# Performance work log

Measured on AMD Instinct MI355X. Metric: run time of the kernel, lower is better.

Reference implementation:

```python
import jax, jax.numpy as jnp
import numpy as np
from functools import partial

EPS = 1e-5
GROUPS = 32
RK4_STEPS = 8


def group_norm(x, g, b):
    B, C, H, W = x.shape
    xr = x.reshape(B, GROUPS, C // GROUPS, H, W)
    m = xr.mean(axis=(2, 3, 4), keepdims=True)
    v = xr.var(axis=(2, 3, 4), keepdims=True)
    xn = ((xr - m) * jax.lax.rsqrt(v + EPS)).reshape(B, C, H, W)
    return xn * g[None, :, None, None] + b[None, :, None, None]


def conv3x3(x, w, b):
    y = jax.lax.conv_general_dilated(x, w, (1, 1), ((1, 1), (1, 1)),
                                     dimension_numbers=('NCHW', 'OIHW', 'NCHW'))
    return y + b[None, :, None, None]


def concat_conv3x3(t, x, w, b):
    # ConcatConv2d: append a constant time channel, then 3x3 conv
    B, _, H, W = x.shape
    tt = jnp.full((B, 1, H, W), t, dtype=x.dtype)
    return conv3x3(jnp.concatenate([tt, x], axis=1), w, b)


def atten_init_fwd(x, p):
    out = jax.nn.relu(group_norm(x, p['ai_g1'], p['ai_b1']))
    out = conv3x3(out, p['ai_w'], p['ai_cb'])
    out = jax.nn.relu(group_norm(out, p['ai_g2'], p['ai_b2']))
    return group_norm(out, p['ai_g3'], p['ai_b3'])


def odefunc(t, x, p):
    out = jax.nn.relu(group_norm(x, p['of_g1'], p['of_b1']))
    out = concat_conv3x3(t, out, p['of_w1'], p['of_cb1'])
    out = jax.nn.relu(group_norm(out, p['of_g2'], p['of_b2']))
    out = concat_conv3x3(t, out, p['of_w2'], p['of_cb2'])
    return group_norm(out, p['of_g3'], p['of_b3'])


def rk4(f, y0, t0, t1, n):
    h = jnp.asarray((t1 - t0) / n, dtype=y0.dtype)
    def step(carry, _):
        y, t = carry
        k1 = f(t, y)
        k2 = f(t + 0.5 * h, y + 0.5 * h * k1)
        k3 = f(t + 0.5 * h, y + 0.5 * h * k2)
        k4 = f(t + h, y + h * k3)
        y = y + (h / 6.0) * (k1 + 2.0 * k2 + 2.0 * k3 + k4)
        return (y, t + h), None
    (y, _), _ = jax.lax.scan(step, (y0, jnp.asarray(t0, y0.dtype)), None, length=n)
    return y


def setup_inputs() -> dict:
    key = jax.random.key(0)
    dim = 32
    B, H, W = 128, 64, 64
    ks = jax.random.split(key, 8)
    d = {
        'x': jax.random.normal(ks[0], (B, dim, H, W), dtype=jnp.float32),
        # atten_init params
        'ai_g1': jnp.ones((dim,), jnp.float32), 'ai_b1': jnp.zeros((dim,), jnp.float32),
        'ai_w': jax.random.normal(ks[1], (dim, dim, 3, 3), jnp.float32) * 0.05,
        'ai_cb': jnp.zeros((dim,), jnp.float32),
        'ai_g2': jnp.ones((dim,), jnp.float32), 'ai_b2': jnp.zeros((dim,), jnp.float32),
        'ai_g3': jnp.ones((dim,), jnp.float32), 'ai_b3': jnp.zeros((dim,), jnp.float32),
        # odefunc params (ConcatConv2d: in_channels = dim + 1 time channel)
        'of_g1': jnp.ones((dim,), jnp.float32), 'of_b1': jnp.zeros((dim,), jnp.float32),
        'of_w1': jax.random.normal(ks[2], (dim, dim + 1, 3, 3), jnp.float32) * 0.05,
        'of_cb1': jnp.zeros((dim,), jnp.float32),
        'of_g2': jnp.ones((dim,), jnp.float32), 'of_b2': jnp.zeros((dim,), jnp.float32),
        'of_w2': jax.random.normal(ks[3], (dim, dim + 1, 3, 3), jnp.float32) * 0.05,
        'of_cb2': jnp.zeros((dim,), jnp.float32),
        'of_g3': jnp.ones((dim,), jnp.float32), 'of_b3': jnp.zeros((dim,), jnp.float32),
    }
    return d


def reference(x, ai_g1, ai_b1, ai_w, ai_cb, ai_g2, ai_b2, ai_g3, ai_b3,
              of_g1, of_b1, of_w1, of_cb1, of_g2, of_b2, of_w2, of_cb2,
              of_g3, of_b3):
    p = dict(ai_g1=ai_g1, ai_b1=ai_b1, ai_w=ai_w, ai_cb=ai_cb, ai_g2=ai_g2,
             ai_b2=ai_b2, ai_g3=ai_g3, ai_b3=ai_b3, of_g1=of_g1, of_b1=of_b1,
             of_w1=of_w1, of_cb1=of_cb1, of_g2=of_g2, of_b2=of_b2, of_w2=of_w2,
             of_cb2=of_cb2, of_g3=of_g3, of_b3=of_b3)
    a0 = atten_init_fwd(x, p)
    x0 = jnp.concatenate([x, a0], axis=0)  # torch.cat default dim=0
    f = lambda t, y: odefunc(t, y, p)
    out1 = rk4(f, x0, 0.0, 1.0, RK4_STEPS)  # odeint(...)[1]
    return out1
```

## Files before the change

kernel.cpp:

```cpp
#include <hip/hip_runtime.h>

#define HW 4096
#define CIN 32

typedef __bf16 bf16x8 __attribute__((ext_vector_type(8)));
typedef float  f32x4  __attribute__((ext_vector_type(4)));
typedef unsigned short ushort8_v __attribute__((ext_vector_type(8)));

__device__ __forceinline__ unsigned short f2b(float f) {
    __bf16 b = (__bf16)f;
    return __builtin_bit_cast(unsigned short, b);
}
__device__ __forceinline__ float b2f(unsigned short s) {
    unsigned int u = ((unsigned int)s) << 16;
    return __builtin_bit_cast(float, u);
}
__device__ __forceinline__ bf16x8 ld_frag(const unsigned short* p) {
    ushort8_v u = *(const ushort8_v*)p;
    return __builtin_bit_cast(bf16x8, u);
}

__global__ __launch_bounds__(256)
void prep_kernel(const float* __restrict__ ai_w,
                 const float* __restrict__ of_w1,
                 const float* __restrict__ of_w2,
                 unsigned short* __restrict__ wp_ai,
                 unsigned short* __restrict__ wp1,
                 unsigned short* __restrict__ wp2,
                 float* __restrict__ tc1, float* __restrict__ tc2)
{
    const int t = threadIdx.x;
    for (int i = t; i < 9 * 32 * 40; i += 256) {
        const int s = i / 1280;
        const int rem = i - s * 1280;
        const int oc = rem / 40;
        const int ci = rem - oc * 40;
        unsigned short va = 0, v1 = 0, v2 = 0;
        if (ci < 32) {
            va = f2b(ai_w[(oc * 32 + ci) * 9 + s]);
            v1 = f2b(of_w1[(oc * 33 + ci + 1) * 9 + s]);
            v2 = f2b(of_w2[(oc * 33 + ci + 1) * 9 + s]);
        }
        wp_ai[i] = va; wp1[i] = v1; wp2[i] = v2;
    }
    for (int i = t; i < 32 * 9; i += 256) {
        const int oc = i / 9;
        const int cls = i - oc * 9;
        const int rc = cls / 3, cc = cls - rc * 3;
        float s1 = 0.f, s2 = 0.f;
        for (int ky = 0; ky < 3; ++ky) {
            if ((rc == 0 && ky == 0) || (rc == 2 && ky == 2)) continue;
            for (int kx = 0; kx < 3; ++kx) {
                if ((cc == 0 && kx == 0) || (cc == 2 && kx == 2)) continue;
                s1 += of_w1[(oc * 33) * 9 + ky * 3 + kx];
                s2 += of_w2[(oc * 33) * 9 + ky * 3 + kx];
            }
        }
        tc1[i] = s1; tc2[i] = s2;
    }
}

__global__ __launch_bounds__(256)
void xstat_kernel(const float* __restrict__ x, float* __restrict__ y,
                  unsigned short* __restrict__ xb,
                  const float* __restrict__ g_ai, const float* __restrict__ b_ai,
                  const float* __restrict__ g_of, const float* __restrict__ b_of,
                  float* __restrict__ st_ai, float* __restrict__ st_of)
{
    const int p = blockIdx.x;
    const int c = p & 31;
    const int t = threadIdx.x;
    const float4* ip = (const float4*)(x + (size_t)p * HW);
    float4* yp = (float4*)(y + (size_t)p * HW);
    ushort4* xp = (ushort4*)(xb + (size_t)p * HW);
    float s = 0.f, ss = 0.f;
#pragma unroll
    for (int i = 0; i < 4; ++i) {
        const float4 q = ip[t + i * 256];
        yp[t + i * 256] = q;
        ushort4 u; u.x = f2b(q.x); u.y = f2b(q.y); u.z = f2b(q.z); u.w = f2b(q.w);
        xp[t + i * 256] = u;
        s += q.x + q.y + q.z + q.w;
        ss += q.x * q.x + q.y * q.y + q.z * q.z + q.w * q.w;
    }
#pragma unroll
    for (int off = 32; off > 0; off >>= 1) {
        s  += __shfl_xor(s, off);
        ss += __shfl_xor(ss, off);
    }
    __shared__ float red[8];
    const int wid = t >> 6;
    if ((t & 63) == 0) { red[wid] = s; red[4 + wid] = ss; }
    __syncthreads();
    if (t == 0) {
        s  = red[0] + red[1] + red[2] + red[3];
        ss = red[4] + red[5] + red[6] + red[7];
        const float mean = s * (1.f / HW);
        const float var  = ss * (1.f / HW) - mean * mean;
        const float rstd = rsqrtf(var + 1e-5f);
        const float sa = g_ai[c] * rstd;
        st_ai[p * 2]     = sa;
        st_ai[p * 2 + 1] = b_ai[c] - mean * sa;
        const float so = g_of[c] * rstd;
        st_of[p * 2]     = so;
        st_of[p * 2 + 1] = b_of[c] - mean * so;
    }
}

template<int HAS_TIME, int STATS, int OUT_BF16, int FIN>
__global__ __launch_bounds__(512)
void conv_kernel(const unsigned short* __restrict__ in, void* __restrict__ outv,
                 const float* __restrict__ st,
                 const float* __restrict__ fg, const float* __restrict__ fb,
                 const unsigned short* __restrict__ wp,
                 const float* __restrict__ cb, const float* __restrict__ tcls,
                 float tval, float* __restrict__ straw)
{
    const int blk = blockIdx.x;
    const int b  = blk >> 3;
    const int hb = blk & 7;
    const int h0 = hb * 8;
    const int t  = threadIdx.x;
    const int l  = t & 63;
    const int wid = t >> 6;
    const int lm = l & 15;
    const int lg = l >> 4;

    __shared__ unsigned short tile[10 * 66 * 40];
    __shared__ float sst[64];

    if (FIN) {
        float s = 0.f, ss = 0.f;
        if (t < 256) {
            const float2 pr = ((const float2*)st)[(size_t)(b * 32 + (t >> 3)) * 8 + (t & 7)];
            s = pr.x; ss = pr.y;
        }
        s += __shfl_xor(s, 1); ss += __shfl_xor(ss, 1);
        s += __shfl_xor(s, 2); ss += __shfl_xor(ss, 2);
        s += __shfl_xor(s, 4); ss += __shfl_xor(ss, 4);
        if (t < 256 && (t & 7) == 0) {
            const int ci = t >> 3;
            const float mean = s * (1.f / HW);
            const float var  = ss * (1.f / HW) - mean * mean;
            const float rstd = rsqrtf(var + 1e-5f);
            const float sc = fg[ci] * rstd;
            sst[ci * 2]     = sc;
            sst[ci * 2 + 1] = fb[ci] - mean * sc;
        }
    } else {
        if (t < 64) sst[t] = st[b * 64 + t];
    }

    bf16x8 wreg[2][9];
    {
        const unsigned short* wb = wp + (size_t)(lm * 40 + 8 * lg);
#pragma unroll
        for (int nt = 0; nt < 2; ++nt)
#pragma unroll
            for (int s = 0; s < 9; ++s)
                wreg[nt][s] = ld_frag(wb + s * 1280 + nt * 640);
    }
    __syncthreads();

    const unsigned short* inb = in + (size_t)b * (CIN * HW);
#pragma unroll
    for (int tau = t; tau < 640; tau += 512) {
        const int g = tau / 160;
        const int rem = tau - g * 160;
        const int r = rem >> 4;
        const int wq = rem & 15;
        const int hh = h0 - 1 + r;
        unsigned short* dst = &tile[(r * 66 + wq * 4 + 1) * 40 + 8 * g];
        if (hh >= 0 && hh < 64) {
            const unsigned short* src = inb + (size_t)(8 * g) * HW + hh * 64 + wq * 4;
            ushort4 U[8];
#pragma unroll
            for (int j = 0; j < 8; ++j) U[j] = *(const ushort4*)(src + (size_t)j * HW);
            float scv[8], shv[8];
#pragma unroll
            for (int j = 0; j < 8; ++j) {
                const float2 s2 = *(const float2*)(&sst[(8 * g + j) * 2]);
                scv[j] = s2.x; shv[j] = s2.y;
            }
#pragma unroll
            for (int k = 0; k < 4; ++k) {
                ushort8_v F;
#pragma unroll
                for (int j = 0; j < 8; ++j) {
                    const unsigned short e = ((const unsigned short*)&U[j])[k];
                    F[j] = f2b(fmaxf(b2f(e) * scv[j] + shv[j], 0.f));
                }
                *(ushort8_v*)(dst + k * 40) = F;
            }
        } else {
            const ushort8_v z = {0, 0, 0, 0, 0, 0, 0, 0};
#pragma unroll
            for (int k = 0; k < 4; ++k) *(ushort8_v*)(dst + k * 40) = z;
        }
    }
    if (t < 80) {
        const int g = t & 3;
        const int rr = t >> 2;
        const int r = rr >> 1;
        const int col = (rr & 1) ? 65 : 0;
        const ushort8_v z = {0, 0, 0, 0, 0, 0, 0, 0};
        *(ushort8_v*)&tile[(r * 66 + col) * 40 + 8 * g] = z;
    }
    __syncthreads();

    f32x4 acc[4][2];
#pragma unroll
    for (int mt = 0; mt < 4; ++mt)
#pragma unroll
        for (int nt = 0; nt < 2; ++nt) acc[mt][nt] = (f32x4){0.f, 0.f, 0.f, 0.f};

#pragma unroll
    for (int ky = 0; ky < 3; ++ky)
#pragma unroll
        for (int kx = 0; kx < 3; ++kx) {
            const int s = ky * 3 + kx;
            const int base = ((wid + ky) * 66 + kx + lm) * 40 + 8 * lg;
#pragma unroll
            for (int mt = 0; mt < 4; ++mt) {
                const bf16x8 a = ld_frag(&tile[base + mt * 640]);
                acc[mt][0] = __builtin_amdgcn_mfma_f32_16x16x32_bf16(a, wreg[0][s], acc[mt][0], 0, 0, 0);
                acc[mt][1] = __builtin_amdgcn_mfma_f32_16x16x32_bf16(a, wreg[1][s], acc[mt][1], 0, 0, 0);
            }
        }

    const int h = h0 + wid;
    const int rc = (h == 0) ? 0 : ((h == 63) ? 2 : 1);
    float bias_[2], tcn[2], tc0[2], tc2[2];
#pragma unroll
    for (int nt = 0; nt < 2; ++nt) {
        const int oc = nt * 16 + lm;
        bias_[nt] = cb[oc];
        if (HAS_TIME) {
            tcn[nt] = tcls[oc * 9 + rc * 3 + 1];
            tc0[nt] = tcls[oc * 9 + rc * 3 + 0];
            tc2[nt] = tcls[oc * 9 + rc * 3 + 2];
        }
    }
    float sl[2] = {0.f, 0.f}, ssl[2] = {0.f, 0.f};
    float* outf = (float*)outv;
    unsigned short* outb = (unsigned short*)outv;
#pragma unroll
    for (int mt = 0; mt < 4; ++mt) {
#pragma unroll
        for (int nt = 0; nt < 2; ++nt) {
            const int oc = nt * 16 + lm;
            float v[4];
#pragma unroll
            for (int r = 0; r < 4; ++r) {
                v[r] = acc[mt][nt][r] + bias_[nt];
                if (HAS_TIME) v[r] += tval * tcn[nt];
            }
            if (HAS_TIME && mt == 0 && lg == 0) v[0] += tval * (tc0[nt] - tcn[nt]);
            if (HAS_TIME && mt == 3 && lg == 3) v[3] += tval * (tc2[nt] - tcn[nt]);
            const int w0 = mt * 16 + lg * 4;
            const size_t o = ((size_t)(b * 32 + oc)) * HW + (size_t)h * 64 + w0;
            if (OUT_BF16) {
                ushort4 u;
                u.x = f2b(v[0]); u.y = f2b(v[1]); u.z = f2b(v[2]); u.w = f2b(v[3]);
                *(ushort4*)&outb[o] = u;
                if (STATS) {
#pragma unroll
                    for (int r = 0; r < 4; ++r) {
                        const float vr = b2f(f2b(v[r]));
                        sl[nt] += vr; ssl[nt] += vr * vr;
                    }
                }
            } else {
                float4 q; q.x = v[0]; q.y = v[1]; q.z = v[2]; q.w = v[3];
                *(float4*)&outf[o] = q;
                if (STATS) {
#pragma unroll
                    for (int r = 0; r < 4; ++r) { sl[nt] += v[r]; ssl[nt] += v[r] * v[r]; }
                }
            }
        }
    }
    if (STATS) {
        float s0 = sl[0], q0 = ssl[0], s1 = sl[1], q1 = ssl[1];
        s0 += __shfl_xor(s0, 16); s0 += __shfl_xor(s0, 32);
        q0 += __shfl_xor(q0, 16); q0 += __shfl_xor(q0, 32);
        s1 += __shfl_xor(s1, 16); s1 += __shfl_xor(s1, 32);
        q1 += __shfl_xor(q1, 16); q1 += __shfl_xor(q1, 32);
        __syncthreads();
        float* red = (float*)tile;
        if (lg == 0) {
            red[wid * 32 + lm]       = s0;  red[256 + wid * 32 + lm]       = q0;
            red[wid * 32 + 16 + lm]  = s1;  red[256 + wid * 32 + 16 + lm]  = q1;
        }
        __syncthreads();
        if (t < 32) {
            float S = 0.f, Q = 0.f;
#pragma unroll
            for (int w = 0; w < 8; ++w) { S += red[w * 32 + t]; Q += red[256 + w * 32 + t]; }
            float* dst = straw + ((size_t)(b * 32 + t) * 8 + hb) * 2;
            dst[0] = S; dst[1] = Q;
        }
    }
}

__global__ __launch_bounds__(256)
void dgn_kernel(const float* __restrict__ in, float* __restrict__ out,
                unsigned short* __restrict__ xbout,
                const float* __restrict__ g2, const float* __restrict__ b2,
                const float* __restrict__ g3, const float* __restrict__ b3,
                const float* __restrict__ g1n, const float* __restrict__ b1n,
                float* __restrict__ stout)
{
    const int p = blockIdx.x;
    const int c = p & 31;
    const int t = threadIdx.x;
    const float4* ip = (const float4*)(in + (size_t)p * HW);
    float4* op = (float4*)(out + (size_t)p * HW);
    ushort4* xp = (ushort4*)(xbout + (size_t)p * HW);
    __shared__ float red[8];
    const int wid = t >> 6;

    float4 v[4];
    float s = 0.f, ss = 0.f;
#pragma unroll
    for (int i = 0; i < 4; ++i) {
        float4 q = ip[t + i * 256];
        v[i] = q;
        s += q.x + q.y + q.z + q.w;
        ss += q.x * q.x + q.y * q.y + q.z * q.z + q.w * q.w;
    }
#pragma unroll
    for (int off = 32; off > 0; off >>= 1) {
        s  += __shfl_xor(s, off);
        ss += __shfl_xor(ss, off);
    }
    if ((t & 63) == 0) { red[wid] = s; red[4 + wid] = ss; }
    __syncthreads();
    s  = red[0] + red[1] + red[2] + red[3];
    ss = red[4] + red[5] + red[6] + red[7];
    float mean = s * (1.f / HW);
    float var  = ss * (1.f / HW) - mean * mean;
    float rstd = rsqrtf(var + 1e-5f);
    float sc = g2[c] * rstd;
    float sh = b2[c] - mean * sc;

    s = 0.f; ss = 0.f;
#pragma unroll
    for (int i = 0; i < 4; ++i) {
        float4 q = v[i];
        q.x = fmaxf(q.x * sc + sh, 0.f); q.y = fmaxf(q.y * sc + sh, 0.f);
        q.z = fmaxf(q.z * sc + sh, 0.f); q.w = fmaxf(q.w * sc + sh, 0.f);
        v[i] = q;
        s += q.x + q.y + q.z + q.w;
        ss += q.x * q.x + q.y * q.y + q.z * q.z + q.w * q.w;
    }
#pragma unroll
    for (int off = 32; off > 0; off >>= 1) {
        s  += __shfl_xor(s, off);
        ss += __shfl_xor(ss, off);
    }
    __syncthreads();
    if ((t & 63) == 0) { red[wid] = s; red[4 + wid] = ss; }
    __syncthreads();
    s  = red[0] + red[1] + red[2] + red[3];
    ss = red[4] + red[5] + red[6] + red[7];
    mean = s * (1.f / HW);
    var  = ss * (1.f / HW) - mean * mean;
    rstd = rsqrtf(var + 1e-5f);
    sc = g3[c] * rstd;
    sh = b3[c] - mean * sc;

    float s3 = 0.f, ss3 = 0.f;
#pragma unroll
    for (int i = 0; i < 4; ++i) {
        float4 q = v[i];
        q.x = q.x * sc + sh; q.y = q.y * sc + sh;
        q.z = q.z * sc + sh; q.w = q.w * sc + sh;
        op[t + i * 256] = q;
        ushort4 u; u.x = f2b(q.x); u.y = f2b(q.y); u.z = f2b(q.z); u.w = f2b(q.w);
        xp[t + i * 256] = u;
        s3 += q.x + q.y + q.z + q.w;
        ss3 += q.x * q.x + q.y * q.y + q.z * q.z + q.w * q.w;
    }
#pragma unroll
    for (int off = 32; off > 0; off >>= 1) {
        s3  += __shfl_xor(s3, off);
        ss3 += __shfl_xor(ss3, off);
    }
    __syncthreads();
    if ((t & 63) == 0) { red[wid] = s3; red[4 + wid] = ss3; }
    __syncthreads();
    if (t == 0) {
        s3  = red[0] + red[1] + red[2] + red[3];
        ss3 = red[4] + red[5] + red[6] + red[7];
        const float m3 = s3 * (1.f / HW);
        const float v3 = ss3 * (1.f / HW) - m3 * m3;
        const float r3 = rsqrtf(v3 + 1e-5f);
        const float sc1 = g1n[c] * r3;
        stout[p * 2]     = sc1;
        stout[p * 2 + 1] = b1n[c] - m3 * sc1;
    }
}

template<int MODE>
__global__ __launch_bounds__(256)
void gnrk_kernel(const unsigned short* __restrict__ kin,
                 const float* __restrict__ straw,
                 const float* __restrict__ g, const float* __restrict__ bt,
                 float* __restrict__ y, float* __restrict__ acc,
                 float ca, float cy,
                 const float* __restrict__ g1n, const float* __restrict__ b1n,
                 float* __restrict__ stout, unsigned short* __restrict__ xb,
                 unsigned short* __restrict__ yb)
{
    const int p = blockIdx.x;
    const int c = p & 31;
    const int t = threadIdx.x;

    const float2 pr = ((const float2*)straw)[(size_t)p * 8 + (t & 7)];
    float s = pr.x, ss = pr.y;
    s += __shfl_xor(s, 1); ss += __shfl_xor(ss, 1);
    s += __shfl_xor(s, 2); ss += __shfl_xor(ss, 2);
    s += __shfl_xor(s, 4); ss += __shfl_xor(ss, 4);
    const float mean = s * (1.f / HW);
    const float var  = ss * (1.f / HW) - mean * mean;
    const float rstd = rsqrtf(var + 1e-5f);
    const float sc = g[c] * rstd;
    const float sh = bt[c] - mean * sc;

    const ushort4* kp = (const ushort4*)(kin + (size_t)p * HW);
    const f32x4* ypl = (const f32x4*)(y + (size_t)p * HW);
    f32x4* yps = (f32x4*)(y + (size_t)p * HW);
    f32x4* ap  = (f32x4*)(acc + (size_t)p * HW);
    ushort4* xp = (ushort4*)(xb + (size_t)p * HW);
    ushort4* ybp = (ushort4*)(yb + (size_t)p * HW);
    __shared__ float red[8];
    const int wid = t >> 6;

    ushort4 ku[4];
#pragma unroll
    for (int i = 0; i < 4; ++i) ku[i] = kp[t + i * 256];
    f32x4 yv[4];
    if (MODE == 0) {
#pragma unroll
        for (int i = 0; i < 4; ++i)
            yv[i] = __builtin_nontemporal_load(ypl + t + i * 256);
    }
    ushort4 ybv[4];
    if (MODE == 1) {
#pragma unroll
        for (int i = 0; i < 4; ++i) ybv[i] = ybp[t + i * 256];
    }
    f32x4 av[4];
    if (MODE != 0) {
#pragma unroll
        for (int i = 0; i < 4; ++i) av[i] = ap[t + i * 256];
    }

    float s2 = 0.f, ss2 = 0.f;
#pragma unroll
    for (int i = 0; i < 4; ++i) {
        const int idx = t + i * 256;
        f32x4 kq;
        kq[0] = b2f(ku[i].x) * sc + sh; kq[1] = b2f(ku[i].y) * sc + sh;
        kq[2] = b2f(ku[i].z) * sc + sh; kq[3] = b2f(ku[i].w) * sc + sh;
        ushort4 u;
        if (MODE == 0) {
            f32x4 a, w;
#pragma unroll
            for (int j = 0; j < 4; ++j) {
                a[j] = yv[i][j] + ca * kq[j];
                w[j] = yv[i][j] + cy * kq[j];
            }
            ap[idx] = a;
            u.x = f2b(w[0]); u.y = f2b(w[1]); u.z = f2b(w[2]); u.w = f2b(w[3]);
            xp[idx] = u;
            ushort4 yu;
            yu.x = f2b(yv[i][0]); yu.y = f2b(yv[i][1]);
            yu.z = f2b(yv[i][2]); yu.w = f2b(yv[i][3]);
            ybp[idx] = yu;
        } else if (MODE == 1) {
            f32x4 a, w;
            a[0] = av[i][0] + ca * kq[0]; a[1] = av[i][1] + ca * kq[1];
            a[2] = av[i][2] + ca * kq[2]; a[3] = av[i][3] + ca * kq[3];
            w[0] = b2f(ybv[i].x) + cy * kq[0]; w[1] = b2f(ybv[i].y) + cy * kq[1];
            w[2] = b2f(ybv[i].z) + cy * kq[2]; w[3] = b2f(ybv[i].w) + cy * kq[3];
            ap[idx] = a;
            u.x = f2b(w[0]); u.y = f2b(w[1]); u.z = f2b(w[2]); u.w = f2b(w[3]);
            xp[idx] = u;
        } else {
            f32x4 w;
            w[0] = av[i][0] + ca * kq[0]; w[1] = av[i][1] + ca * kq[1];
            w[2] = av[i][2] + ca * kq[2]; w[3] = av[i][3] + ca * kq[3];
            __builtin_nontemporal_store(w, yps + idx);
            u.x = f2b(w[0]); u.y = f2b(w[1]); u.z = f2b(w[2]); u.w = f2b(w[3]);
            xp[idx] = u;
        }
        const float r0 = b2f(u.x), r1 = b2f(u.y), r2 = b2f(u.z), r3 = b2f(u.w);
        s2  += r0 + r1 + r2 + r3;
        ss2 += r0 * r0 + r1 * r1 + r2 * r2 + r3 * r3;
    }
#pragma unroll
    for (int off = 32; off > 0; off >>= 1) {
        s2  += __shfl_xor(s2, off);
        ss2 += __shfl_xor(ss2, off);
    }
    if ((t & 63) == 0) { red[wid] = s2; red[4 + wid] = ss2; }
    __syncthreads();
    if (t == 0) {
        s2  = red[0] + red[1] + red[2] + red[3];
        ss2 = red[4] + red[5] + red[6] + red[7];
        const float m2 = s2 * (1.f / HW);
        const float v2 = ss2 * (1.f / HW) - m2 * m2;
        const float r2 = rsqrtf(v2 + 1e-5f);
        const float sc1 = g1n[c] * r2;
        stout[p * 2]     = sc1;
        stout[p * 2 + 1] = b1n[c] - m2 * sc1;
    }
}

extern "C" void kernel_launch(void* const* d_in, const int* in_sizes, int n_in,
                              void* d_out, int out_size, void* d_ws, size_t ws_size,
                              hipStream_t stream) {
    (void)in_sizes; (void)n_in; (void)out_size; (void)ws_size;
    const float* x      = (const float*)d_in[0];
    const float* ai_g1  = (const float*)d_in[1];
    const float* ai_b1  = (const float*)d_in[2];
    const float* ai_w   = (const float*)d_in[3];
    const float* ai_cb  = (const float*)d_in[4];
    const float* ai_g2  = (const float*)d_in[5];
    const float* ai_b2  = (const float*)d_in[6];
    const float* ai_g3  = (const float*)d_in[7];
    const float* ai_b3  = (const float*)d_in[8];
    const float* of_g1  = (const float*)d_in[9];
    const float* of_b1  = (const float*)d_in[10];
    const float* of_w1  = (const float*)d_in[11];
    const float* of_cb1 = (const float*)d_in[12];
    const float* of_g2  = (const float*)d_in[13];
    const float* of_b2  = (const float*)d_in[14];
    const float* of_w2  = (const float*)d_in[15];
    const float* of_cb2 = (const float*)d_in[16];
    const float* of_g3  = (const float*)d_in[17];
    const float* of_b3  = (const float*)d_in[18];

    float* y = (float*)d_out;
    const size_t N  = (size_t)256 * 32 * 64 * 64;
    const size_t NH = N / 2;
    float* ws = (float*)d_ws;
    float* ACC = ws;
    float* YTf = ws;
    unsigned short* Abf = (unsigned short*)(ws + N);
    unsigned short* XB  = (unsigned short*)(ws + N + N / 2);
    unsigned short* YTB = (unsigned short*)(ws + 2 * N);
    unsigned short* YB  = (unsigned short*)(ws + 2 * N + N / 2);
    float* tail  = ws + 3 * N;
    float* ST1    = tail;               tail += 16384;
    float* ST_AI  = tail;               tail += 8192;
    float* STRAW1 = tail;               tail += 131072;
    float* STRAW2 = tail;               tail += 131072;
    unsigned short* WPai = (unsigned short*)tail;  tail += 5760;
    unsigned short* WP1  = (unsigned short*)tail;  tail += 5760;
    unsigned short* WP2  = (unsigned short*)tail;  tail += 5760;
    float* TC1  = tail;                 tail += 288;
    float* TC2  = tail;                 tail += 288;

    const float h = 0.125f;

    prep_kernel<<<1, 256, 0, stream>>>(ai_w, of_w1, of_w2, WPai, WP1, WP2, TC1, TC2);

    xstat_kernel<<<4096, 256, 0, stream>>>(x, y, XB, ai_g1, ai_b1, of_g1, of_b1,
                                           ST_AI, ST1);
    conv_kernel<0, 0, 0, 0><<<1024, 512, 0, stream>>>(XB, YTf, ST_AI, nullptr, nullptr,
                                                      WPai, ai_cb, nullptr, 0.f, nullptr);
    dgn_kernel<<<4096, 256, 0, stream>>>(YTf, y + NH, XB + NH, ai_g2, ai_b2,
                                         ai_g3, ai_b3, of_g1, of_b1, ST1 + 8192);

    auto eval = [&](float tv, float ca, float cy, int mode) {
        conv_kernel<1, 1, 1, 0><<<2048, 512, 0, stream>>>(XB, Abf, ST1, nullptr, nullptr,
                                                          WP1, of_cb1, TC1, tv, STRAW1);
        conv_kernel<1, 1, 1, 1><<<2048, 512, 0, stream>>>(Abf, YTB, STRAW1, of_g2, of_b2,
                                                          WP2, of_cb2, TC2, tv, STRAW2);
        if (mode == 0)
            gnrk_kernel<0><<<8192, 256, 0, stream>>>(YTB, STRAW2, of_g3, of_b3, y, ACC,
                                                     ca, cy, of_g1, of_b1, ST1, XB, YB);
        else if (mode == 1)
            gnrk_kernel<1><<<8192, 256, 0, stream>>>(YTB, STRAW2, of_g3, of_b3, y, ACC,
                                                     ca, cy, of_g1, of_b1, ST1, XB, YB);
        else
            gnrk_kernel<2><<<8192, 256, 0, stream>>>(YTB, STRAW2, of_g3, of_b3, y, ACC,
                                                     ca, cy, of_g1, of_b1, ST1, XB, YB);
    };

    for (int s = 0; s < 8; ++s) {
        const float t0 = h * (float)s;
        eval(t0,            h / 6.f, 0.5f * h, 0);
        eval(t0 + 0.5f * h, h / 3.f, 0.5f * h, 1);
        eval(t0 + 0.5f * h, h / 3.f, h,        1);
        eval(t0 + h,        h / 6.f, 0.f,      2);
    }
}
```

Measured before the change: 5.493 ms.

## Store RK4 increment accumulator in bf16 and keep y bf16 copy from prior step

The RK4 accumulator moves from an fp32 buffer holding y+sum to a bf16 buffer holding only the weighted sum of k terms, with y added back in fp32 at the final stage. The bf16 copy of y is now produced by the previous final stage (and by the init kernels) instead of in mode 0. Mode 0 no longer reads the fp32 y, so only mode 2 touches fp32 y, which cuts global memory traffic in the bandwidth-bound elementwise kernels and shrinks the workspace. In exchange, increments are rounded to bf16 in the accumulator, which risks accuracy.

```diff
diff --git a/kernel.cpp b/kernel.cpp
--- a/kernel.cpp
+++ b/kernel.cpp
@@ -62,7 +62,7 @@
 
 __global__ __launch_bounds__(256)
 void xstat_kernel(const float* __restrict__ x, float* __restrict__ y,
-                  unsigned short* __restrict__ xb,
+                  unsigned short* __restrict__ xb, unsigned short* __restrict__ yb,
                   const float* __restrict__ g_ai, const float* __restrict__ b_ai,
                   const float* __restrict__ g_of, const float* __restrict__ b_of,
                   float* __restrict__ st_ai, float* __restrict__ st_of)
@@ -73,6 +73,7 @@
     const float4* ip = (const float4*)(x + (size_t)p * HW);
     float4* yp = (float4*)(y + (size_t)p * HW);
     ushort4* xp = (ushort4*)(xb + (size_t)p * HW);
+    ushort4* ybp = (ushort4*)(yb + (size_t)p * HW);
     float s = 0.f, ss = 0.f;
 #pragma unroll
     for (int i = 0; i < 4; ++i) {
@@ -80,6 +81,7 @@
         yp[t + i * 256] = q;
         ushort4 u; u.x = f2b(q.x); u.y = f2b(q.y); u.z = f2b(q.z); u.w = f2b(q.w);
         xp[t + i * 256] = u;
+        ybp[t + i * 256] = u;
         s += q.x + q.y + q.z + q.w;
         ss += q.x * q.x + q.y * q.y + q.z * q.z + q.w * q.w;
     }
@@ -305,7 +307,7 @@
 
 __global__ __launch_bounds__(256)
 void dgn_kernel(const float* __restrict__ in, float* __restrict__ out,
-                unsigned short* __restrict__ xbout,
+                unsigned short* __restrict__ xbout, unsigned short* __restrict__ ybout,
                 const float* __restrict__ g2, const float* __restrict__ b2,
                 const float* __restrict__ g3, const float* __restrict__ b3,
                 const float* __restrict__ g1n, const float* __restrict__ b1n,
@@ -317,6 +319,7 @@
     const float4* ip = (const float4*)(in + (size_t)p * HW);
     float4* op = (float4*)(out + (size_t)p * HW);
     ushort4* xp = (ushort4*)(xbout + (size_t)p * HW);
+    ushort4* ybp = (ushort4*)(ybout + (size_t)p * HW);
     __shared__ float red[8];
     const int wid = t >> 6;
 
@@ -379,6 +382,7 @@
         op[t + i * 256] = q;
         ushort4 u; u.x = f2b(q.x); u.y = f2b(q.y); u.z = f2b(q.z); u.w = f2b(q.w);
         xp[t + i * 256] = u;
+        ybp[t + i * 256] = u;
         s3 += q.x + q.y + q.z + q.w;
         ss3 += q.x * q.x + q.y * q.y + q.z * q.z + q.w * q.w;
     }
@@ -407,7 +411,7 @@
 void gnrk_kernel(const unsigned short* __restrict__ kin,
                  const float* __restrict__ straw,
                  const float* __restrict__ g, const float* __restrict__ bt,
-                 float* __restrict__ y, float* __restrict__ acc,
+                 float* __restrict__ y, unsigned short* __restrict__ db,
                  float ca, float cy,
                  const float* __restrict__ g1n, const float* __restrict__ b1n,
                  float* __restrict__ stout, unsigned short* __restrict__ xb,
@@ -431,8 +435,8 @@
     const ushort4* kp = (const ushort4*)(kin + (size_t)p * HW);
     const f32x4* ypl = (const f32x4*)(y + (size_t)p * HW);
     f32x4* yps = (f32x4*)(y + (size_t)p * HW);
-    f32x4* ap  = (f32x4*)(acc + (size_t)p * HW);
-    ushort4* xp = (ushort4*)(xb + (size_t)p * HW);
+    ushort4* dp  = (ushort4*)(db + (size_t)p * HW);
+    ushort4* xp  = (ushort4*)(xb + (size_t)p * HW);
     ushort4* ybp = (ushort4*)(yb + (size_t)p * HW);
     __shared__ float red[8];
     const int wid = t >> 6;
@@ -440,21 +444,21 @@
     ushort4 ku[4];
 #pragma unroll
     for (int i = 0; i < 4; ++i) ku[i] = kp[t + i * 256];
+    ushort4 ybv[4];
+    if (MODE != 2) {
+#pragma unroll
+        for (int i = 0; i < 4; ++i) ybv[i] = ybp[t + i * 256];
+    }
+    ushort4 dv[4];
+    if (MODE != 0) {
+#pragma unroll
+        for (int i = 0; i < 4; ++i) dv[i] = dp[t + i * 256];
+    }
     f32x4 yv[4];
-    if (MODE == 0) {
+    if (MODE == 2) {
 #pragma unroll
         for (int i = 0; i < 4; ++i)
             yv[i] = __builtin_nontemporal_load(ypl + t + i * 256);
-    }
-    ushort4 ybv[4];
-    if (MODE == 1) {
-#pragma unroll
-        for (int i = 0; i < 4; ++i) ybv[i] = ybp[t + i * 256];
-    }
-    f32x4 av[4];
-    if (MODE != 0) {
-#pragma unroll
-        for (int i = 0; i < 4; ++i) av[i] = ap[t + i * 256];
     }
 
     float s2 = 0.f, ss2 = 0.f;
@@ -465,36 +469,32 @@
         kq[0] = b2f(ku[i].x) * sc + sh; kq[1] = b2f(ku[i].y) * sc + sh;
         kq[2] = b2f(ku[i].z) * sc + sh; kq[3] = b2f(ku[i].w) * sc + sh;
         ushort4 u;
-        if (MODE == 0) {
-            f32x4 a, w;
-#pragma unroll
-            for (int j = 0; j < 4; ++j) {
-                a[j] = yv[i][j] + ca * kq[j];
-                w[j] = yv[i][j] + cy * kq[j];
+        if (MODE != 2) {
+            f32x4 d, w;
+            if (MODE == 0) {
+#pragma unroll
+                for (int j = 0; j < 4; ++j) d[j] = ca * kq[j];
+            } else {
+                d[0] = b2f(dv[i].x) + ca * kq[0]; d[1] = b2f(dv[i].y) + ca * kq[1];
+                d[2] = b2f(dv[i].z) + ca * kq[2]; d[3] = b2f(dv[i].w) + ca * kq[3];
             }
-            ap[idx] = a;
-            u.x = f2b(w[0]); u.y = f2b(w[1]); u.z = f2b(w[2]); u.w = f2b(w[3]);
-            xp[idx] = u;
-            ushort4 yu;
-            yu.x = f2b(yv[i][0]); yu.y = f2b(yv[i][1]);
-            yu.z = f2b(yv[i][2]); yu.w = f2b(yv[i][3]);
-            ybp[idx] = yu;
-        } else if (MODE == 1) {
-            f32x4 a, w;
-            a[0] = av[i][0] + ca * kq[0]; a[1] = av[i][1] + ca * kq[1];
-            a[2] = av[i][2] + ca * kq[2]; a[3] = av[i][3] + ca * kq[3];
             w[0] = b2f(ybv[i].x) + cy * kq[0]; w[1] = b2f(ybv[i].y) + cy * kq[1];
             w[2] = b2f(ybv[i].z) + cy * kq[2]; w[3] = b2f(ybv[i].w) + cy * kq[3];
-            ap[idx] = a;
+            ushort4 du;
+            du.x = f2b(d[0]); du.y = f2b(d[1]); du.z = f2b(d[2]); du.w = f2b(d[3]);
+            dp[idx] = du;
             u.x = f2b(w[0]); u.y = f2b(w[1]); u.z = f2b(w[2]); u.w = f2b(w[3]);
             xp[idx] = u;
         } else {
             f32x4 w;
-            w[0] = av[i][0] + ca * kq[0]; w[1] = av[i][1] + ca * kq[1];
-            w[2] = av[i][2] + ca * kq[2]; w[3] = av[i][3] + ca * kq[3];
+            w[0] = yv[i][0] + b2f(dv[i].x) + ca * kq[0];
+            w[1] = yv[i][1] + b2f(dv[i].y) + ca * kq[1];
+            w[2] = yv[i][2] + b2f(dv[i].z) + ca * kq[2];
+            w[3] = yv[i][3] + b2f(dv[i].w) + ca * kq[3];
             __builtin_nontemporal_store(w, yps + idx);
             u.x = f2b(w[0]); u.y = f2b(w[1]); u.z = f2b(w[2]); u.w = f2b(w[3]);
             xp[idx] = u;
+            ybp[idx] = u;
         }
         const float r0 = b2f(u.x), r1 = b2f(u.y), r2 = b2f(u.z), r3 = b2f(u.w);
         s2  += r0 + r1 + r2 + r3;
@@ -547,13 +547,13 @@
     const size_t N  = (size_t)256 * 32 * 64 * 64;
     const size_t NH = N / 2;
     float* ws = (float*)d_ws;
-    float* ACC = ws;
+    unsigned short* DB  = (unsigned short*)ws;
     float* YTf = ws;
+    unsigned short* YB  = (unsigned short*)(ws + N / 2);
     unsigned short* Abf = (unsigned short*)(ws + N);
     unsigned short* XB  = (unsigned short*)(ws + N + N / 2);
     unsigned short* YTB = (unsigned short*)(ws + 2 * N);
-    unsigned short* YB  = (unsigned short*)(ws + 2 * N + N / 2);
-    float* tail  = ws + 3 * N;
+    float* tail  = ws + 2 * N + N / 2;
     float* ST1    = tail;               tail += 16384;
     float* ST_AI  = tail;               tail += 8192;
     float* STRAW1 = tail;               tail += 131072;
@@ -568,11 +568,11 @@
 
     prep_kernel<<<1, 256, 0, stream>>>(ai_w, of_w1, of_w2, WPai, WP1, WP2, TC1, TC2);
 
-    xstat_kernel<<<4096, 256, 0, stream>>>(x, y, XB, ai_g1, ai_b1, of_g1, of_b1,
+    xstat_kernel<<<4096, 256, 0, stream>>>(x, y, XB, YB, ai_g1, ai_b1, of_g1, of_b1,
                                            ST_AI, ST1);
     conv_kernel<0, 0, 0, 0><<<1024, 512, 0, stream>>>(XB, YTf, ST_AI, nullptr, nullptr,
                                                       WPai, ai_cb, nullptr, 0.f, nullptr);
-    dgn_kernel<<<4096, 256, 0, stream>>>(YTf, y + NH, XB + NH, ai_g2, ai_b2,
+    dgn_kernel<<<4096, 256, 0, stream>>>(YTf, y + NH, XB + NH, YB + NH, ai_g2, ai_b2,
                                          ai_g3, ai_b3, of_g1, of_b1, ST1 + 8192);
 
     auto eval = [&](float tv, float ca, float cy, int mode) {
@@ -581,13 +581,13 @@
         conv_kernel<1, 1, 1, 1><<<2048, 512, 0, stream>>>(Abf, YTB, STRAW1, of_g2, of_b2,
                                                           WP2, of_cb2, TC2, tv, STRAW2);
         if (mode == 0)
-            gnrk_kernel<0><<<8192, 256, 0, stream>>>(YTB, STRAW2, of_g3, of_b3, y, ACC,
+            gnrk_kernel<0><<<8192, 256, 0, stream>>>(YTB, STRAW2, of_g3, of_b3, y, DB,
                                                      ca, cy, of_g1, of_b1, ST1, XB, YB);
         else if (mode == 1)
-            gnrk_kernel<1><<<8192, 256, 0, stream>>>(YTB, STRAW2, of_g3, of_b3, y, ACC,
+            gnrk_kernel<1><<<8192, 256, 0, stream>>>(YTB, STRAW2, of_g3, of_b3, y, DB,
                                                      ca, cy, of_g1, of_b1, ST1, XB, YB);
         else
-            gnrk_kernel<2><<<8192, 256, 0, stream>>>(YTB, STRAW2, of_g3, of_b3, y, ACC,
+            gnrk_kernel<2><<<8192, 256, 0, stream>>>(YTB, STRAW2, of_g3, of_b3, y, DB,
                                                      ca, cy, of_g1, of_b1, ST1, XB, YB);
     };
 
```

Result: faster. 4.898 ms (-10.8%).
